# Optimization experiments

Measured on AMD Instinct MI355X. Metric: run time of the kernel, lower is better.

The kernel has to match this reference:

```python
import jax, jax.numpy as jnp
import numpy as np

N = 40000
IN_DIM = 2000
HID = 512
OUT_DIM = 30
E = 400000


def setup_inputs() -> dict:
    key = jax.random.key(0)
    k1, k2, k3, k4, k5, k6 = jax.random.split(key, 6)
    features = jax.random.normal(k1, (N, IN_DIM), dtype=jnp.float32)
    edge_index = jax.random.randint(k2, (2, E), 0, N, dtype=jnp.int64)
    # xavier_normal_(gain=1.414): std = gain * sqrt(2/(fan_in+fan_out))
    W1 = jax.random.normal(k3, (IN_DIM, HID), dtype=jnp.float32) * (1.414 * np.sqrt(2.0 / (IN_DIM + HID)))
    W2 = jax.random.normal(k4, (HID, OUT_DIM), dtype=jnp.float32) * (1.414 * np.sqrt(2.0 / (HID + OUT_DIM)))
    att_src = jax.random.normal(k5, (HID,), dtype=jnp.float32) * (1.414 * np.sqrt(2.0 / (1 + HID)))
    att_dst = jax.random.normal(k6, (HID,), dtype=jnp.float32) * (1.414 * np.sqrt(2.0 / (1 + HID)))
    return {"features": features, "W1": W1, "W2": W2,
            "att_src": att_src, "att_dst": att_dst, "edge_index": edge_index}


def _gat_propagate(x_proj, alpha_src, alpha_dst, src, dst, n_nodes):
    """GATConv message+aggregate (heads=1, aggr='add').
    x_proj: [N, C] projected features; alpha_src/alpha_dst: [N] per-node scores.
    """
    score = jax.nn.sigmoid(alpha_src[src] + alpha_dst[dst])          # [E]
    # segment softmax over destination neighborhoods (PyG softmax)
    seg_max = jax.ops.segment_max(score, dst, num_segments=n_nodes)  # [N]
    e = jnp.exp(score - seg_max[dst])                                # [E]
    seg_sum = jax.ops.segment_sum(e, dst, num_segments=n_nodes)     # [N]
    alpha = e / (seg_sum[dst] + 1e-16)                               # [E]
    msg = x_proj[src] * alpha[:, None]                               # [E, C] gather + scale
    return jax.ops.segment_sum(msg, dst, num_segments=n_nodes)      # [N, C] scatter-add


def _stagate_forward(features, W1, W2, att_src, att_dst, src, dst):
    n = features.shape[0]
    # conv1: attention=True (computes its own alpha)
    x1 = features @ W1                                # [N, HID]
    a_src = x1 @ att_src                              # [N]
    a_dst = x1 @ att_dst                              # [N]
    h1 = jax.nn.elu(_gat_propagate(x1, a_src, a_dst, src, dst, n))
    # conv2: attention=False -> just linear projection (heads=1 mean)
    h2 = h1 @ W2                                      # [N, OUT_DIM]
    # conv3: weights tied to W2^T, attention tied to conv1's alphas
    x3 = h2 @ W2.T                                    # [N, HID]
    h3 = jax.nn.elu(_gat_propagate(x3, a_src, a_dst, src, dst, n))
    # conv4: attention=False, weights tied to W1^T
    h4 = h3 @ W1.T                                    # [N, IN_DIM]
    return h2, h4


def reference(features, W1, W2, att_src, att_dst, edge_index):
    src = edge_index[0]
    dst = edge_index[1]
    return _stagate_forward(features, W1, W2, att_src, att_dst, src, dst)
```

## Files before the change

### kernel.cpp

```cpp
#include <hip/hip_runtime.h>
#include <cstdint>

#define NNODES 40000
#define INDIM 2000
#define HIDD 512
#define ODIM 30
#define NEDGES 400000
#define KPAD 2048
#define ROWSPLIT 20224

typedef short bf16x8 __attribute__((ext_vector_type(8)));
typedef float f32x4 __attribute__((ext_vector_type(4)));

__device__ __forceinline__ float bf2f(ushort u){ union{unsigned int i; float f;} x; x.i = ((unsigned int)u)<<16; return x.f; }
__device__ __forceinline__ ushort f2bf(float v){ union{float f; unsigned int u;} x; x.f=v; unsigned int r = x.u + 0x7fffu + ((x.u>>16)&1u); return (ushort)(r>>16); }

__device__ __forceinline__ int xcd_swz(int orig, int nwg){
  int q = nwg >> 3, r = nwg & 7;
  int xcd = orig & 7;
  int idx = orig >> 3;
  return (xcd < r ? xcd*(q+1) : r*(q+1) + (xcd-r)*q) + idx;
}

#define P_MID  asm volatile("" ::: "memory"); __builtin_amdgcn_s_barrier(); \
               asm volatile("s_waitcnt lgkmcnt(0)" ::: "memory"); \
               __builtin_amdgcn_sched_barrier(0); __builtin_amdgcn_s_setprio(1);
#define P_END  __builtin_amdgcn_s_setprio(0); asm volatile("" ::: "memory"); \
               __builtin_amdgcn_s_barrier(); __builtin_amdgcn_sched_barrier(0);
#define P_ENDW __builtin_amdgcn_s_setprio(0); \
               asm volatile("s_waitcnt vmcnt(4)" ::: "memory"); \
               asm volatile("" ::: "memory"); __builtin_amdgcn_s_barrier(); \
               __builtin_amdgcn_sched_barrier(0);

template<typename OutT>
__device__ __forceinline__ void gemm_body(
    const ushort* __restrict__ A, const ushort* __restrict__ Bt,
    OutT* __restrict__ C, int M, int N, int K, int ldc,
    int row0, int col0, char* smem)
{
  ushort* Al = (ushort*)smem;
  ushort* Bl = (ushort*)(smem + 65536);
  const int tid = threadIdx.x;
  const int lane = tid & 63;
  const int w = tid >> 6;
  const int wm = w >> 2, wn = w & 3;
  const int NT = K >> 6;

  f32x4 acc[8][4] = {};
  bf16x8 a[4][2], b[4][2];

  auto stage = [&](bool isA, int kt, int h){
    const ushort* G = isA ? A : Bt;
    int base = isA ? row0 : col0;
    int lim  = isA ? M : N;
    ushort* L = (isA ? Al : Bl) + ((kt & 1) << 14);
    if (kt >= NT) kt -= NT;
    #pragma unroll
    for (int it = 0; it < 2; ++it){
      int ch = tid + (it << 9);
      int rl = (h << 7) + (ch >> 3);
      int cs = ch & 7;
      int gr = base + rl; gr = gr < lim ? gr : lim - 1;
      int gc = (kt << 6) + ((cs ^ (rl & 7)) << 3);
      __builtin_amdgcn_global_load_lds(
        (const __attribute__((address_space(1))) unsigned int*)(G + (size_t)gr*K + gc),
        (__attribute__((address_space(3))) unsigned int*)(L + rl*64 + cs*8), 16, 0, 0);
    }
  };
  auto lda = [&](int buf, int mf, int kk) -> bf16x8 {
    int rl = wm*128 + mf*16 + (lane & 15);
    int ko = kk*32 + ((lane >> 4) << 3);
    return *(const bf16x8*)&Al[(buf << 14) + rl*64 + (ko ^ ((rl & 7) << 3))];
  };
  auto ldb = [&](int buf, int nf, int kk) -> bf16x8 {
    int rl = wn*64 + nf*16 + (lane & 15);
    int ko = kk*32 + ((lane >> 4) << 3);
    return *(const bf16x8*)&Bl[(buf << 14) + rl*64 + (ko ^ ((rl & 7) << 3))];
  };
  auto mfma_q = [&](int mbase, int nbase){
    #pragma unroll
    for (int i=0;i<4;++i)
      #pragma unroll
      for (int j=0;j<2;++j)
        #pragma unroll
        for (int kk=0;kk<2;++kk)
          acc[mbase+i][nbase+j] = __builtin_amdgcn_mfma_f32_16x16x32_bf16(
              a[i][kk], b[nbase+j][kk], acc[mbase+i][nbase+j], 0, 0, 0);
  };

  stage(false, 0, 0); stage(false, 0, 1);
  stage(true , 0, 0); stage(true , 0, 1);
  stage(false, 1, 0); stage(false, 1, 1);
  asm volatile("s_waitcnt vmcnt(4)" ::: "memory");
  asm volatile("" ::: "memory");
  __builtin_amdgcn_s_barrier();
  __builtin_amdgcn_sched_barrier(0);

  const int NT2 = NT >> 1;
  for (int t = 0; t < NT2; ++t){
    const int kt0 = 2*t, kt1 = 2*t + 1;
    #pragma unroll
    for (int i=0;i<4;++i){ a[i][0]=lda(0,i,0); a[i][1]=lda(0,i,1); }
    #pragma unroll
    for (int j=0;j<2;++j){ b[j][0]=ldb(0,j,0); b[j][1]=ldb(0,j,1); }
    stage(true, kt1, 0);
    P_MID; mfma_q(0,0); P_END;
    #pragma unroll
    for (int j=2;j<4;++j){ b[j][0]=ldb(0,j,0); b[j][1]=ldb(0,j,1); }
    stage(true, kt1, 1);
    P_MID; mfma_q(0,2); P_END;
    #pragma unroll
    for (int i=0;i<4;++i){ a[i][0]=lda(0,4+i,0); a[i][1]=lda(0,4+i,1); }
    stage(false, kt0+2, 0);
    P_MID; mfma_q(4,0); P_END;
    stage(false, kt0+2, 1);
    P_MID; mfma_q(4,2); P_ENDW;
    #pragma unroll
    for (int i=0;i<4;++i){ a[i][0]=lda(1,i,0); a[i][1]=lda(1,i,1); }
    #pragma unroll
    for (int j=0;j<2;++j){ b[j][0]=ldb(1,j,0); b[j][1]=ldb(1,j,1); }
    stage(true, kt0+2, 0);
    P_MID; mfma_q(0,0); P_END;
    #pragma unroll
    for (int j=2;j<4;++j){ b[j][0]=ldb(1,j,0); b[j][1]=ldb(1,j,1); }
    stage(true, kt0+2, 1);
    P_MID; mfma_q(0,2); P_END;
    #pragma unroll
    for (int i=0;i<4;++i){ a[i][0]=lda(1,4+i,0); a[i][1]=lda(1,4+i,1); }
    stage(false, kt1+2, 0);
    P_MID; mfma_q(4,0); P_END;
    stage(false, kt1+2, 1);
    P_MID; mfma_q(4,2); P_ENDW;
  }

  asm volatile("s_waitcnt vmcnt(0)" ::: "memory");
  __syncthreads();

  if constexpr (sizeof(OutT)==2) {
    ushort* cs = (ushort*)smem;
    #pragma unroll
    for (int p=0;p<2;++p){
      if (wm == p){
        #pragma unroll
        for (int mf=0;mf<8;++mf)
          #pragma unroll
          for (int nf=0;nf<4;++nf)
            #pragma unroll
            for (int reg=0;reg<4;++reg)
              cs[(mf*16 + ((lane>>4)<<2) + reg)*264 + wn*64 + nf*16 + (lane&15)] = f2bf(acc[mf][nf][reg]);
      }
      __syncthreads();
      #pragma unroll
      for (int it=0; it<8; ++it){
        int ch = tid + it*512;
        int r = ch >> 5, c8 = (ch & 31) * 8;
        int gr = row0 + p*128 + r;
        if (gr < M && col0 + c8 + 8 <= N)
          *(bf16x8*)&((ushort*)C)[(size_t)gr*ldc + col0 + c8] = *(const bf16x8*)&cs[r*264 + c8];
      }
      __syncthreads();
    }
  } else {
    float* cf = (float*)smem;
    #pragma unroll
    for (int p=0;p<4;++p){
      if (wm == (p>>1)){
        int mh = (p & 1) * 4;
        #pragma unroll
        for (int i=0;i<4;++i)
          #pragma unroll
          for (int nf=0;nf<4;++nf)
            #pragma unroll
            for (int reg=0;reg<4;++reg)
              cf[(i*16 + ((lane>>4)<<2) + reg)*260 + wn*64 + nf*16 + (lane&15)] = acc[mh+i][nf][reg];
      }
      __syncthreads();
      #pragma unroll
      for (int it=0; it<8; ++it){
        int ch = tid + it*512;
        int r = ch >> 6, c4 = (ch & 63) * 4;
        int gr = row0 + p*64 + r, gc = col0 + c4;
        if (gr < M && gc + 4 <= N)
          __builtin_nontemporal_store(*(const f32x4*)&cf[r*260 + c4],
                                      (f32x4*)&((float*)C)[(size_t)gr*ldc + gc]);
      }
      __syncthreads();
    }
  }
}

__device__ __forceinline__ void cast_rows2(const float* __restrict__ features,
    ushort* __restrict__ featb, int row_base, int cb){
  int t = threadIdx.x;
  int row = row_base + (cb<<1) + (t>>8);
  int kc = t & 255;
  bf16x8 o;
  if (kc < INDIM/8) {
    const float* p = features + (size_t)row*INDIM + kc*8;
    #pragma unroll
    for (int j=0;j<8;++j) o[j] = (short)f2bf(p[j]);
  } else {
    #pragma unroll
    for (int j=0;j<8;++j) o[j] = 0;
  }
  *(bf16x8*)(featb + (size_t)row*KPAD + kc*8) = o;
}

__device__ __forceinline__ void scan_body(const int* __restrict__ degp,
    int* __restrict__ row_ptr, int* part){
  const int t = threadIdx.x;
  const int base = t * 80;
  int s = 0;
  for (int j=0;j<80;++j){ int i = base+j; s += (i < NNODES) ? degp[i] : 0; }
  part[t] = s;
  __syncthreads();
  for (int off=1; off<512; off<<=1){
    int x = (t >= off) ? part[t-off] : 0;
    __syncthreads();
    part[t] += x;
    __syncthreads();
  }
  int run = (t > 0) ? part[t-1] : 0;
  for (int j=0;j<80;++j){
    int i = base+j;
    if (i <= NNODES){
      row_ptr[i] = run;
      if (i < NNODES) run += degp[i];
    }
  }
}

#define S1_CAST   10112
#define S1_W1     (S1_CAST + 2000)
#define S1_W2     (S1_W1 + 32)
#define S1_HIST   (S1_W2 + 782)
#define S1_PAD    (S1_HIST + 48)
#define S1_CUR    (S1_PAD + 79)

__global__ __launch_bounds__(512) void setup_kernel(
    const float* __restrict__ features, const float* __restrict__ W1, const float* __restrict__ W2,
    const int* __restrict__ edst,
    ushort* __restrict__ featb, ushort* __restrict__ W1b, ushort* __restrict__ W1t,
    ushort* __restrict__ W2p, ushort* __restrict__ W2tc,
    int* __restrict__ deg, int* __restrict__ cursor){
  int b = blockIdx.x, t = threadIdx.x;
  if (b < S1_CAST){
    cast_rows2(features, featb, 0, b);
  } else if (b < S1_W1){
    int idx = (b - S1_CAST)*512 + t;
    int r = idx >> 9, c = idx & 511;
    ushort bb = f2bf(W1[idx]);
    W1b[idx] = bb;
    W1t[(size_t)c*KPAD + r] = bb;
  } else if (b < S1_W2){
    int idx = (b - S1_W1)*512 + t;
    int k = idx >> 5, c = idx & 31;
    float val = (c < ODIM) ? W2[k*ODIM + c] : 0.f;
    ushort bb = f2bf(val);
    W2p[k*32 + c] = bb;
    W2tc[c*HIDD + k] = bb;
  } else if (b < S1_HIST){
    int e = (b - S1_W2)*512 + t;
    if (e < NEDGES) atomicAdd(&deg[edst[e]], 1);
  } else if (b < S1_PAD){
    int z = (b - S1_HIST)*512 + t;
    int c = z / 48, r = 2000 + (z - c*48);
    W1t[(size_t)c*KPAD + r] = 0;
  } else {
    int z = (b - S1_PAD)*512 + t;
    if (z < NNODES) cursor[z] = 0;
  }
}

#define K2_G 158
__global__ __launch_bounds__(512, 2) void gemm1a_kernel(
    const ushort* __restrict__ featb, const ushort* __restrict__ W1t, ushort* __restrict__ x1,
    const float* __restrict__ features, ushort* __restrict__ featb_w,
    const int* __restrict__ deg, int* __restrict__ row_ptr){
  __shared__ __align__(16) char smem[131072];
  int b = blockIdx.x;
  if (b < K2_G){
    int s = xcd_swz(b, K2_G);
    int row0 = (s >> 1) << 8;
    int col0 = (s & 1) << 8;
    gemm_body<ushort>(featb, W1t, x1, NNODES, HIDD, KPAD, HIDD, row0, col0, smem);
  } else if (b == K2_G){
    scan_body(deg, row_ptr, (int*)smem);
  } else {
    cast_rows2(features, featb_w, ROWSPLIT, b - K2_G - 1);
  }
}

#define K3_G 156
#define K3_PL (K3_G + 782)
__global__ __launch_bounds__(512, 2) void gemm1b_kernel(
    const ushort* __restrict__ featb, const ushort* __restrict__ W1t, ushort* __restrict__ x1,
    const int* __restrict__ esrc, const int* __restrict__ edst,
    const int* __restrict__ row_ptr, int* __restrict__ cursor, int* __restrict__ csr_src,
    const float* __restrict__ att_src, const float* __restrict__ att_dst,
    float* __restrict__ a_src, float* __restrict__ a_dst){
  __shared__ __align__(16) char smem[131072];
  int b = blockIdx.x, t = threadIdx.x;
  if (b < K3_G){
    int s = xcd_swz(b, K3_G);
    int row0 = ROWSPLIT + ((s >> 1) << 8);
    int col0 = (s & 1) << 8;
    gemm_body<ushort>(featb, W1t, x1, NNODES, HIDD, KPAD, HIDD, row0, col0, smem);
  } else if (b < K3_PL){
    int e = (b - K3_G)*512 + t;
    if (e < NEDGES){
      int d = edst[e];
      int pos = row_ptr[d] + atomicAdd(&cursor[d], 1);
      csr_src[pos] = esrc[e];
    }
  } else {
    int gid = (b - K3_PL)*512 + t;
    int row = gid >> 6, lane = gid & 63;
    bf16x8 v = *(const bf16x8*)(x1 + (size_t)row*HIDD + lane*8);
    float ps = 0.f, pd = 0.f;
    #pragma unroll
    for (int j=0;j<8;++j){
      float xv = bf2f((ushort)v[j]);
      ps += xv * att_src[lane*8+j];
      pd += xv * att_dst[lane*8+j];
    }
    #pragma unroll
    for (int off=32; off>0; off>>=1){ ps += __shfl_down(ps, off); pd += __shfl_down(pd, off); }
    if (lane == 0){ a_src[row] = ps; a_dst[row] = pd; }
  }
}

__global__ __launch_bounds__(512) void a2_kernel(const ushort* __restrict__ x1,
    const float* __restrict__ att_src, const float* __restrict__ att_dst,
    float* __restrict__ a_src, float* __restrict__ a_dst){
  int gid = blockIdx.x*512 + threadIdx.x;
  int row = ROWSPLIT + (gid >> 6), lane = gid & 63;
  if (row >= NNODES) return;
  bf16x8 v = *(const bf16x8*)(x1 + (size_t)row*HIDD + lane*8);
  float ps = 0.f, pd = 0.f;
  #pragma unroll
  for (int j=0;j<8;++j){
    float xv = bf2f((ushort)v[j]);
    ps += xv * att_src[lane*8+j];
    pd += xv * att_dst[lane*8+j];
  }
  #pragma unroll
  for (int off=32; off>0; off>>=1){ ps += __shfl_down(ps, off); pd += __shfl_down(pd, off); }
  if (lane == 0){ a_src[row] = ps; a_dst[row] = pd; }
}

__global__ __launch_bounds__(256) void alpha_kernel(const int* __restrict__ row_ptr,
    const int* __restrict__ csr_src, const float* __restrict__ a_src,
    const float* __restrict__ a_dst, float* __restrict__ csr_alpha){
  int gid = blockIdx.x*256 + threadIdx.x;
  int v = gid >> 4, lane = gid & 15;
  if (v >= NNODES) return;
  int p0 = row_ptr[v], p1 = row_ptr[v+1];
  if (p0 >= p1) return;
  float ad = a_dst[v];
  float m = -1e30f;
  for (int p = p0 + lane; p < p1; p += 16){
    float s = 1.f/(1.f + __expf(-(a_src[csr_src[p]] + ad)));
    m = fmaxf(m, s);
  }
  #pragma unroll
  for (int off=8; off>0; off>>=1) m = fmaxf(m, __shfl_xor(m, off));
  float sum = 0.f;
  for (int p = p0 + lane; p < p1; p += 16){
    float s = 1.f/(1.f + __expf(-(a_src[csr_src[p]] + ad)));
    float e = __expf(s - m);
    csr_alpha[p] = e;
    sum += e;
  }
  #pragma unroll
  for (int off=8; off>0; off>>=1) sum += __shfl_xor(sum, off);
  float inv = 1.f/(sum + 1e-16f);
  for (int p = p0 + lane; p < p1; p += 16) csr_alpha[p] *= inv;
}

__global__ __launch_bounds__(256) void agg1_kernel(const ushort* __restrict__ X,
    const int* __restrict__ row_ptr, const int* __restrict__ csr_src,
    const float* __restrict__ csr_alpha, ushort* __restrict__ outb){
  int gid = blockIdx.x*256 + threadIdx.x;
  int v = gid >> 6, lane = gid & 63;
  if (v >= NNODES) return;
  int p0 = __builtin_amdgcn_readfirstlane(row_ptr[v]);
  int p1 = __builtin_amdgcn_readfirstlane(row_ptr[v+1]);
  float acc[8] = {0.f,0.f,0.f,0.f,0.f,0.f,0.f,0.f};
  int p = p0;
  for (; p + 8 <= p1; p += 8){
    int s[8]; float A[8];
    #pragma unroll
    for (int u=0;u<8;++u){ s[u] = csr_src[p+u]; A[u] = csr_alpha[p+u]; }
    bf16x8 x[8];
    #pragma unroll
    for (int u=0;u<8;++u) x[u] = *(const bf16x8*)(X + (size_t)s[u]*HIDD + lane*8);
    #pragma unroll
    for (int u=0;u<8;++u)
      #pragma unroll
      for (int k=0;k<8;++k) acc[k] += A[u] * bf2f((ushort)x[u][k]);
  }
  for (; p + 4 <= p1; p += 4){
    int s0 = csr_src[p], s1 = csr_src[p+1], s2 = csr_src[p+2], s3 = csr_src[p+3];
    float A0 = csr_alpha[p], A1 = csr_alpha[p+1], A2 = csr_alpha[p+2], A3 = csr_alpha[p+3];
    bf16x8 x0 = *(const bf16x8*)(X + (size_t)s0*HIDD + lane*8);
    bf16x8 x1 = *(const bf16x8*)(X + (size_t)s1*HIDD + lane*8);
    bf16x8 x2 = *(const bf16x8*)(X + (size_t)s2*HIDD + lane*8);
    bf16x8 x3 = *(const bf16x8*)(X + (size_t)s3*HIDD + lane*8);
    #pragma unroll
    for (int k=0;k<8;++k)
      acc[k] += A0*bf2f((ushort)x0[k]) + A1*bf2f((ushort)x1[k])
              + A2*bf2f((ushort)x2[k]) + A3*bf2f((ushort)x3[k]);
  }
  for (; p < p1; ++p){
    int sj = csr_src[p];
    float aj = csr_alpha[p];
    bf16x8 xv = *(const bf16x8*)(X + (size_t)sj*HIDD + lane*8);
    #pragma unroll
    for (int k=0;k<8;++k) acc[k] += aj * bf2f((ushort)xv[k]);
  }
  bf16x8 o;
  #pragma unroll
  for (int k=0;k<8;++k){
    float a = acc[k];
    a = a > 0.f ? a : __expf(a)-1.f;
    o[k] = (short)f2bf(a);
  }
  *(bf16x8*)(outb + (size_t)v*HIDD + lane*8) = o;
}

__global__ __launch_bounds__(256) void mid_kernel(const ushort* __restrict__ h1,
    const ushort* __restrict__ W2tc, float* __restrict__ h2){
  __shared__ ushort h1s[32*512];
  __shared__ ushort w2s[32*512];
  const int t = threadIdx.x;
  const int row0 = blockIdx.x * 32;
  const ushort* g = h1 + (size_t)row0*HIDD;
  #pragma unroll
  for (int it=0; it<8; ++it){
    int ch = t + it*256;
    *(bf16x8*)&h1s[ch*8] = *(const bf16x8*)&g[ch*8];
    *(bf16x8*)&w2s[ch*8] = *(const bf16x8*)&W2tc[ch*8];
  }
  __syncthreads();
  int c = t & 31, rg = t >> 5;
  if (c < ODIM){
    float acc[4] = {0.f,0.f,0.f,0.f};
    for (int k0=0;k0<64;++k0){
      bf16x8 wv = *(const bf16x8*)&w2s[c*512 + k0*8];
      #pragma unroll
      for (int rr=0; rr<4; ++rr){
        bf16x8 hv = *(const bf16x8*)&h1s[(rg*4+rr)*HIDD + k0*8];
        #pragma unroll
        for (int j=0;j<8;++j) acc[rr] += bf2f((ushort)hv[j]) * bf2f((ushort)wv[j]);
      }
    }
    #pragma unroll
    for (int rr=0;rr<4;++rr) h2[(size_t)(row0 + rg*4 + rr)*ODIM + c] = acc[rr];
  }
}

__global__ __launch_bounds__(256) void conv3_kernel(const float* __restrict__ h2,
    const int* __restrict__ row_ptr, const int* __restrict__ csr_src,
    const float* __restrict__ csr_alpha, const ushort* __restrict__ W2p,
    ushort* __restrict__ h3){
  int gid = blockIdx.x*256 + threadIdx.x;
  int v = gid >> 6, lane = gid & 63;
  if (v >= NNODES) return;
  int p0 = __builtin_amdgcn_readfirstlane(row_ptr[v]);
  int p1 = __builtin_amdgcn_readfirstlane(row_ptr[v+1]);
  float accd = 0.f;
  if (lane < ODIM){
    int p = p0;
    for (; p + 4 <= p1; p += 4){
      int s0 = csr_src[p], s1 = csr_src[p+1], s2 = csr_src[p+2], s3 = csr_src[p+3];
      float a0 = csr_alpha[p], a1 = csr_alpha[p+1], a2 = csr_alpha[p+2], a3 = csr_alpha[p+3];
      accd += a0*h2[(size_t)s0*ODIM + lane] + a1*h2[(size_t)s1*ODIM + lane]
            + a2*h2[(size_t)s2*ODIM + lane] + a3*h2[(size_t)s3*ODIM + lane];
    }
    for (; p < p1; ++p)
      accd += csr_alpha[p] * h2[(size_t)csr_src[p]*ODIM + lane];
  }
  float gv[ODIM];
  #pragma unroll
  for (int ci=0; ci<ODIM; ++ci) gv[ci] = __shfl(accd, ci);
  #pragma unroll
  for (int it=0; it<8; ++it){
    int n = it*64 + lane;
    const ushort* wrp = W2p + n*32;
    bf16x8 wvv[4];
    #pragma unroll
    for (int qd=0;qd<4;++qd) wvv[qd] = *(const bf16x8*)(wrp + qd*8);
    float acc = 0.f;
    #pragma unroll
    for (int ci=0; ci<ODIM; ++ci) acc += gv[ci]*bf2f((ushort)wvv[ci>>3][ci&7]);
    acc = acc > 0.f ? acc : __expf(acc)-1.f;
    h3[(size_t)v*HIDD + n] = f2bf(acc);
  }
}

template<typename OutT>
__global__ __launch_bounds__(512, 2) void gemm8_kernel(
    const ushort* __restrict__ A, const ushort* __restrict__ Bt,
    OutT* __restrict__ C, int M, int N, int K, int ldc, int nwg, int cshift)
{
  __shared__ __align__(16) char smem[131072];
  int s = xcd_swz(blockIdx.x, nwg);
  int row0 = (s >> cshift) << 8;
  int col0 = (s & ((1 << cshift) - 1)) << 8;
  gemm_body<OutT>(A, Bt, C, M, N, K, ldc, row0, col0, smem);
}

extern "C" void kernel_launch(void* const* d_in, const int* in_sizes, int n_in,
                              void* d_out, int out_size, void* d_ws, size_t ws_size,
                              hipStream_t stream){
  const float* features = (const float*)d_in[0];
  const float* W1 = (const float*)d_in[1];
  const float* W2 = (const float*)d_in[2];
  const float* att_src = (const float*)d_in[3];
  const float* att_dst = (const float*)d_in[4];
  const int* edge = (const int*)d_in[5];
  const int* esrc = edge;
  const int* edst = edge + NEDGES;

  float* h2 = (float*)d_out;
  float* h4 = h2 + (size_t)NNODES*ODIM;
  char* obase = (char*)h4;
  ushort* featb = (ushort*)obase;
  ushort* x1b   = (ushort*)(obase + 163840000);
  ushort* h1b   = (ushort*)(obase + 204800000);

  char* wbase = (char*)d_ws;
  size_t o = 0;
  auto walloc = [&](size_t bytes)->void*{ void* p = wbase + o; o += (bytes + 255) & ~(size_t)255; return p; };
  ushort* h3b      = (ushort*)walloc((size_t)NNODES*HIDD*2);
  ushort* W1b      = (ushort*)walloc((size_t)INDIM*HIDD*2);
  ushort* W1t      = (ushort*)walloc((size_t)HIDD*KPAD*2);
  ushort* W2p      = (ushort*)walloc(512*32*2);
  ushort* W2tc     = (ushort*)walloc(32*512*2);
  float*  a_src    = (float*)walloc(NNODES*4);
  float*  a_dst    = (float*)walloc(NNODES*4);
  int*    deg      = (int*)walloc(NNODES*4);
  int*    cursor   = (int*)walloc(NNODES*4);
  int*    row_ptr  = (int*)walloc((NNODES+1)*4);
  int*    csr_src  = (int*)walloc(NEDGES*4);
  float*  csr_alpha= (float*)walloc(NEDGES*4);

  hipMemsetAsync(deg, 0, NNODES*4, stream);

  setup_kernel<<<S1_CUR, 512, 0, stream>>>(features, W1, W2, edst,
      featb, W1b, W1t, W2p, W2tc, deg, cursor);

  gemm1a_kernel<<<K2_G + 1 + 9888, 512, 0, stream>>>(featb, W1t, x1b,
      features, featb, deg, row_ptr);

  gemm1b_kernel<<<K3_PL + 2528, 512, 0, stream>>>(featb, W1t, x1b,
      esrc, edst, row_ptr, cursor, csr_src, att_src, att_dst, a_src, a_dst);

  a2_kernel<<<2472, 512, 0, stream>>>(x1b, att_src, att_dst, a_src, a_dst);

  alpha_kernel<<<2500, 256, 0, stream>>>(row_ptr, csr_src, a_src, a_dst, csr_alpha);

  agg1_kernel<<<10000, 256, 0, stream>>>(x1b, row_ptr, csr_src, csr_alpha, h1b);
  mid_kernel<<<NNODES/32, 256, 0, stream>>>(h1b, W2tc, h2);
  conv3_kernel<<<10000, 256, 0, stream>>>(h2, row_ptr, csr_src, csr_alpha, W2p, h3b);
  gemm8_kernel<float><<<1256, 512, 0, stream>>>(h3b, W1b, h4,
      NNODES, INDIM, HIDD, INDIM, 1256, 3);
}
```

Before: 570.9 us.

## Split alpha and agg1 by node range to overlap aggregation with attention

Splits the attention-softmax and first aggregation into two node halves. A combined kernel runs aggregation on the first half while computing alpha for the second half, followed by a separate aggregation kernel for the second half. This is meant to hide the latency-bound alpha pass behind gather work, at the cost of an extra launch. Also switches the feature cast to vectorized nontemporal float4 loads.

```diff
diff --git a/kernel.cpp b/kernel.cpp
--- a/kernel.cpp
+++ b/kernel.cpp
@@ -8,6 +8,7 @@
 #define NEDGES 400000
 #define KPAD 2048
 #define ROWSPLIT 20224
+#define ASPLIT 20480
 
 typedef short bf16x8 __attribute__((ext_vector_type(8)));
 typedef float f32x4 __attribute__((ext_vector_type(4)));
@@ -196,9 +197,13 @@
   int kc = t & 255;
   bf16x8 o;
   if (kc < INDIM/8) {
-    const float* p = features + (size_t)row*INDIM + kc*8;
-    #pragma unroll
-    for (int j=0;j<8;++j) o[j] = (short)f2bf(p[j]);
+    const f32x4* p = (const f32x4*)(features + (size_t)row*INDIM + kc*8);
+    f32x4 lo = __builtin_nontemporal_load(p);
+    f32x4 hi = __builtin_nontemporal_load(p+1);
+    #pragma unroll
+    for (int j=0;j<4;++j) o[j] = (short)f2bf(lo[j]);
+    #pragma unroll
+    for (int j=0;j<4;++j) o[4+j] = (short)f2bf(hi[j]);
   } else {
     #pragma unroll
     for (int j=0;j<8;++j) o[j] = 0;
@@ -228,6 +233,87 @@
       if (i < NNODES) run += degp[i];
     }
   }
+}
+
+__device__ __forceinline__ void alpha_body(int b, int voff,
+    const int* __restrict__ row_ptr, const int* __restrict__ csr_src,
+    const float* __restrict__ a_src, const float* __restrict__ a_dst,
+    float* __restrict__ csr_alpha){
+  int gid = b*256 + threadIdx.x;
+  int v = voff + (gid >> 4), lane = gid & 15;
+  if (v >= NNODES) return;
+  int p0 = row_ptr[v], p1 = row_ptr[v+1];
+  if (p0 >= p1) return;
+  float ad = a_dst[v];
+  float m = -1e30f;
+  for (int p = p0 + lane; p < p1; p += 16){
+    float s = 1.f/(1.f + __expf(-(a_src[csr_src[p]] + ad)));
+    m = fmaxf(m, s);
+  }
+  #pragma unroll
+  for (int off=8; off>0; off>>=1) m = fmaxf(m, __shfl_xor(m, off));
+  float sum = 0.f;
+  for (int p = p0 + lane; p < p1; p += 16){
+    float s = 1.f/(1.f + __expf(-(a_src[csr_src[p]] + ad)));
+    float e = __expf(s - m);
+    csr_alpha[p] = e;
+    sum += e;
+  }
+  #pragma unroll
+  for (int off=8; off>0; off>>=1) sum += __shfl_xor(sum, off);
+  float inv = 1.f/(sum + 1e-16f);
+  for (int p = p0 + lane; p < p1; p += 16) csr_alpha[p] *= inv;
+}
+
+__device__ __forceinline__ void agg1_body(int b, int voff, const ushort* __restrict__ X,
+    const int* __restrict__ row_ptr, const int* __restrict__ csr_src,
+    const float* __restrict__ csr_alpha, ushort* __restrict__ outb){
+  int gid = b*256 + threadIdx.x;
+  int v = voff + (gid >> 6), lane = gid & 63;
+  if (v >= NNODES) return;
+  int p0 = __builtin_amdgcn_readfirstlane(row_ptr[v]);
+  int p1 = __builtin_amdgcn_readfirstlane(row_ptr[v+1]);
+  float acc[8] = {0.f,0.f,0.f,0.f,0.f,0.f,0.f,0.f};
+  int p = p0;
+  for (; p + 8 <= p1; p += 8){
+    int s[8]; float A[8];
+    #pragma unroll
+    for (int u=0;u<8;++u){ s[u] = csr_src[p+u]; A[u] = csr_alpha[p+u]; }
+    bf16x8 x[8];
+    #pragma unroll
+    for (int u=0;u<8;++u) x[u] = *(const bf16x8*)(X + (size_t)s[u]*HIDD + lane*8);
+    #pragma unroll
+    for (int u=0;u<8;++u)
+      #pragma unroll
+      for (int k=0;k<8;++k) acc[k] += A[u] * bf2f((ushort)x[u][k]);
+  }
+  for (; p + 4 <= p1; p += 4){
+    int s0 = csr_src[p], s1 = csr_src[p+1], s2 = csr_src[p+2], s3 = csr_src[p+3];
+    float A0 = csr_alpha[p], A1 = csr_alpha[p+1], A2 = csr_alpha[p+2], A3 = csr_alpha[p+3];
+    bf16x8 x0 = *(const bf16x8*)(X + (size_t)s0*HIDD + lane*8);
+    bf16x8 x1 = *(const bf16x8*)(X + (size_t)s1*HIDD + lane*8);
+    bf16x8 x2 = *(const bf16x8*)(X + (size_t)s2*HIDD + lane*8);
+    bf16x8 x3 = *(const bf16x8*)(X + (size_t)s3*HIDD + lane*8);
+    #pragma unroll
+    for (int k=0;k<8;++k)
+      acc[k] += A0*bf2f((ushort)x0[k]) + A1*bf2f((ushort)x1[k])
+              + A2*bf2f((ushort)x2[k]) + A3*bf2f((ushort)x3[k]);
+  }
+  for (; p < p1; ++p){
+    int sj = csr_src[p];
+    float aj = csr_alpha[p];
+    bf16x8 xv = *(const bf16x8*)(X + (size_t)sj*HIDD + lane*8);
+    #pragma unroll
+    for (int k=0;k<8;++k) acc[k] += aj * bf2f((ushort)xv[k]);
+  }
+  bf16x8 o;
+  #pragma unroll
+  for (int k=0;k<8;++k){
+    float a = acc[k];
+    a = a > 0.f ? a : __expf(a)-1.f;
+    o[k] = (short)f2bf(a);
+  }
+  *(bf16x8*)(outb + (size_t)v*HIDD + lane*8) = o;
 }
 
 #define S1_CAST   10112
@@ -349,84 +435,29 @@
   if (lane == 0){ a_src[row] = ps; a_dst[row] = pd; }
 }
 
-__global__ __launch_bounds__(256) void alpha_kernel(const int* __restrict__ row_ptr,
+__global__ __launch_bounds__(256) void alpha_a_kernel(const int* __restrict__ row_ptr,
     const int* __restrict__ csr_src, const float* __restrict__ a_src,
     const float* __restrict__ a_dst, float* __restrict__ csr_alpha){
-  int gid = blockIdx.x*256 + threadIdx.x;
-  int v = gid >> 4, lane = gid & 15;
-  if (v >= NNODES) return;
-  int p0 = row_ptr[v], p1 = row_ptr[v+1];
-  if (p0 >= p1) return;
-  float ad = a_dst[v];
-  float m = -1e30f;
-  for (int p = p0 + lane; p < p1; p += 16){
-    float s = 1.f/(1.f + __expf(-(a_src[csr_src[p]] + ad)));
-    m = fmaxf(m, s);
-  }
-  #pragma unroll
-  for (int off=8; off>0; off>>=1) m = fmaxf(m, __shfl_xor(m, off));
-  float sum = 0.f;
-  for (int p = p0 + lane; p < p1; p += 16){
-    float s = 1.f/(1.f + __expf(-(a_src[csr_src[p]] + ad)));
-    float e = __expf(s - m);
-    csr_alpha[p] = e;
-    sum += e;
-  }
-  #pragma unroll
-  for (int off=8; off>0; off>>=1) sum += __shfl_xor(sum, off);
-  float inv = 1.f/(sum + 1e-16f);
-  for (int p = p0 + lane; p < p1; p += 16) csr_alpha[p] *= inv;
-}
-
-__global__ __launch_bounds__(256) void agg1_kernel(const ushort* __restrict__ X,
+  alpha_body(blockIdx.x, 0, row_ptr, csr_src, a_src, a_dst, csr_alpha);
+}
+
+#define OV_AGG (ASPLIT/4)
+__global__ __launch_bounds__(256) void ov_kernel(const ushort* __restrict__ X,
+    const int* __restrict__ row_ptr, const int* __restrict__ csr_src,
+    float* __restrict__ csr_alpha, ushort* __restrict__ outb,
+    const float* __restrict__ a_src, const float* __restrict__ a_dst){
+  int b = blockIdx.x;
+  if (b < OV_AGG){
+    agg1_body(b, 0, X, row_ptr, csr_src, csr_alpha, outb);
+  } else {
+    alpha_body(b - OV_AGG, ASPLIT, row_ptr, csr_src, a_src, a_dst, csr_alpha);
+  }
+}
+
+__global__ __launch_bounds__(256) void agg1b_kernel(const ushort* __restrict__ X,
     const int* __restrict__ row_ptr, const int* __restrict__ csr_src,
     const float* __restrict__ csr_alpha, ushort* __restrict__ outb){
-  int gid = blockIdx.x*256 + threadIdx.x;
-  int v = gid >> 6, lane = gid & 63;
-  if (v >= NNODES) return;
-  int p0 = __builtin_amdgcn_readfirstlane(row_ptr[v]);
-  int p1 = __builtin_amdgcn_readfirstlane(row_ptr[v+1]);
-  float acc[8] = {0.f,0.f,0.f,0.f,0.f,0.f,0.f,0.f};
-  int p = p0;
-  for (; p + 8 <= p1; p += 8){
-    int s[8]; float A[8];
-    #pragma unroll
-    for (int u=0;u<8;++u){ s[u] = csr_src[p+u]; A[u] = csr_alpha[p+u]; }
-    bf16x8 x[8];
-    #pragma unroll
-    for (int u=0;u<8;++u) x[u] = *(const bf16x8*)(X + (size_t)s[u]*HIDD + lane*8);
-    #pragma unroll
-    for (int u=0;u<8;++u)
-      #pragma unroll
-      for (int k=0;k<8;++k) acc[k] += A[u] * bf2f((ushort)x[u][k]);
-  }
-  for (; p + 4 <= p1; p += 4){
-    int s0 = csr_src[p], s1 = csr_src[p+1], s2 = csr_src[p+2], s3 = csr_src[p+3];
-    float A0 = csr_alpha[p], A1 = csr_alpha[p+1], A2 = csr_alpha[p+2], A3 = csr_alpha[p+3];
-    bf16x8 x0 = *(const bf16x8*)(X + (size_t)s0*HIDD + lane*8);
-    bf16x8 x1 = *(const bf16x8*)(X + (size_t)s1*HIDD + lane*8);
-    bf16x8 x2 = *(const bf16x8*)(X + (size_t)s2*HIDD + lane*8);
-    bf16x8 x3 = *(const bf16x8*)(X + (size_t)s3*HIDD + lane*8);
-    #pragma unroll
-    for (int k=0;k<8;++k)
-      acc[k] += A0*bf2f((ushort)x0[k]) + A1*bf2f((ushort)x1[k])
-              + A2*bf2f((ushort)x2[k]) + A3*bf2f((ushort)x3[k]);
-  }
-  for (; p < p1; ++p){
-    int sj = csr_src[p];
-    float aj = csr_alpha[p];
-    bf16x8 xv = *(const bf16x8*)(X + (size_t)sj*HIDD + lane*8);
-    #pragma unroll
-    for (int k=0;k<8;++k) acc[k] += aj * bf2f((ushort)xv[k]);
-  }
-  bf16x8 o;
-  #pragma unroll
-  for (int k=0;k<8;++k){
-    float a = acc[k];
-    a = a > 0.f ? a : __expf(a)-1.f;
-    o[k] = (short)f2bf(a);
-  }
-  *(bf16x8*)(outb + (size_t)v*HIDD + lane*8) = o;
+  agg1_body(blockIdx.x, ASPLIT, X, row_ptr, csr_src, csr_alpha, outb);
 }
 
 __global__ __launch_bounds__(256) void mid_kernel(const ushort* __restrict__ h1,
@@ -559,9 +590,13 @@
 
   a2_kernel<<<2472, 512, 0, stream>>>(x1b, att_src, att_dst, a_src, a_dst);
 
-  alpha_kernel<<<2500, 256, 0, stream>>>(row_ptr, csr_src, a_src, a_dst, csr_alpha);
-
-  agg1_kernel<<<10000, 256, 0, stream>>>(x1b, row_ptr, csr_src, csr_alpha, h1b);
+  alpha_a_kernel<<<ASPLIT*16/256, 256, 0, stream>>>(row_ptr, csr_src, a_src, a_dst, csr_alpha);
+
+  ov_kernel<<<OV_AGG + (NNODES-ASPLIT)*16/256, 256, 0, stream>>>(x1b, row_ptr, csr_src,
+      csr_alpha, h1b, a_src, a_dst);
+
+  agg1b_kernel<<<(NNODES-ASPLIT)/4, 256, 0, stream>>>(x1b, row_ptr, csr_src, csr_alpha, h1b);
+
   mid_kernel<<<NNODES/32, 256, 0, stream>>>(h1b, W2tc, h2);
   conv3_kernel<<<10000, 256, 0, stream>>>(h2, row_ptr, csr_src, csr_alpha, W2p, h3b);
   gemm8_kernel<float><<<1256, 512, 0, stream>>>(h3b, W1b, h4,
```

New measurement: 570.5 us. No clear change (-0.1%).
